# Optimization experiments

Measured on AMD Instinct MI355X. Metric: run time of the kernel, lower is better.

The kernel has to match this reference:

```python
import jax, jax.numpy as jnp
from jax import lax
import numpy as np

DIM = 512
NUM_HEADS = 8
SR = 2


def setup_inputs() -> dict:
    key = jax.random.key(0)
    ks = jax.random.split(key, 7)
    B, H, W = 4, 64, 64
    N = H * W
    C = DIM
    s = 0.02
    return {
        "x": jax.random.normal(ks[0], (B, N, C), dtype=jnp.float32),
        "q_w": jax.random.normal(ks[1], (C, C), dtype=jnp.float32) * s,
        "kv_w": jax.random.normal(ks[2], (2 * C, C), dtype=jnp.float32) * s,
        "sr_w": jax.random.normal(ks[3], (C, C, SR, SR), dtype=jnp.float32) * s,
        "sr_b": jax.random.normal(ks[4], (C,), dtype=jnp.float32) * s,
        "proj_w": jax.random.normal(ks[5], (C, C), dtype=jnp.float32) * s,
        "proj_b": jax.random.normal(ks[6], (C,), dtype=jnp.float32) * s,
        "H": H,
        "W": W,
    }


def reference(x, q_w, kv_w, sr_w, sr_b, proj_w, proj_b, H, W):
    B, N, C = x.shape
    nh = NUM_HEADS
    hd = C // nh
    scale = hd ** -0.5

    # q projection: [B, nh, N, hd]
    q = (x @ q_w.T).reshape(B, N, nh, hd).transpose(0, 2, 1, 3)

    # spatial reduction via strided conv (kernel=stride=SR)
    x_ = x.transpose(0, 2, 1).reshape(B, C, H, W)
    x_ = lax.conv_general_dilated(
        x_, sr_w, window_strides=(SR, SR), padding="VALID",
        dimension_numbers=("NCHW", "OIHW", "NCHW"),
    ) + sr_b[None, :, None, None]
    Nk = (H // SR) * (W // SR)
    x_ = x_.reshape(B, C, Nk).transpose(0, 2, 1)  # [B, Nk, C]

    # kv projection: [2, B, nh, Nk, hd]
    kv = (x_ @ kv_w.T).reshape(B, Nk, 2, nh, hd).transpose(2, 0, 3, 1, 4)
    k, v = kv[0], kv[1]

    attn = jax.nn.softmax(jnp.einsum("bhnd,bhmd->bhnm", q, k) * scale, axis=-1)
    out = jnp.einsum("bhnm,bhmd->bhnd", attn, v)  # [B, nh, N, hd]
    out = out.transpose(0, 2, 1, 3).reshape(B, N, C)
    return out @ proj_w.T + proj_b
```

## Files before the change

### kernel.cpp

```cpp
#include <hip/hip_runtime.h>


typedef __attribute__((ext_vector_type(8)))  short short8;
typedef __attribute__((ext_vector_type(8)))  unsigned short ushort8;
typedef __attribute__((ext_vector_type(4)))  float floatx4;
typedef __attribute__((ext_vector_type(16))) float floatx16;

__device__ inline unsigned short bf16r(float f) {
    union { float f; unsigned u; } v; v.f = f;
    unsigned r = v.u + 0x7fffu + ((v.u >> 16) & 1u);
    return (unsigned short)(r >> 16);
}

__device__ inline unsigned long long pack4ull(float4 v) {
    return (unsigned long long)bf16r(v.x)
         | ((unsigned long long)bf16r(v.y) << 16)
         | ((unsigned long long)bf16r(v.z) << 32)
         | ((unsigned long long)bf16r(v.w) << 48);
}

__device__ inline ushort8 pack8(float4 a, float4 b) {
    ushort8 o;
    o[0] = bf16r(a.x); o[1] = bf16r(a.y); o[2] = bf16r(a.z); o[3] = bf16r(a.w);
    o[4] = bf16r(b.x); o[5] = bf16r(b.y); o[6] = bf16r(b.z); o[7] = bf16r(b.w);
    return o;
}

__device__ inline void gl_lds16(const void* g, void* l) {
    __builtin_amdgcn_global_load_lds(
        (const __attribute__((address_space(1))) unsigned int*)g,
        (__attribute__((address_space(3))) unsigned int*)l, 16, 0, 0);
}

__global__ __launch_bounds__(256)
void prep(const float* __restrict__ x,  const float* __restrict__ qw,
          const float* __restrict__ kvw, const float* __restrict__ srw,
          const float* __restrict__ pw,
          unsigned short* __restrict__ xb,  unsigned short* __restrict__ qwb,
          unsigned short* __restrict__ kvwb, unsigned short* __restrict__ srwb,
          unsigned short* __restrict__ pwb, unsigned short* __restrict__ xrb) {
    const int bid = blockIdx.x;
    if (bid < 2048) {
        const int id = bid * 256 + threadIdx.x;
        const int cq = id & 127, m = id >> 7;
        const int c0 = cq * 4;
        const int b = m >> 10, rem = m & 1023;
        const int oi = rem >> 5, oj = rem & 31;
        const int n00 = oi * 128 + oj * 2;
        const float* bp = x + ((size_t)(b * 4096 + n00)) * 512 + c0;
        const float4 r00 = *(const float4*)bp;
        const float4 r01 = *(const float4*)(bp + 512);
        const float4 r10 = *(const float4*)(bp + 64 * 512);
        const float4 r11 = *(const float4*)(bp + 65 * 512);
        const unsigned long long w00 = pack4ull(r00), w01 = pack4ull(r01),
                                 w10 = pack4ull(r10), w11 = pack4ull(r11);
        unsigned short* xo = xb + ((size_t)(b * 4096 + n00)) * 512 + c0;
        *(unsigned long long*)(xo)            = w00;
        *(unsigned long long*)(xo + 512)      = w01;
        *(unsigned long long*)(xo + 64 * 512) = w10;
        *(unsigned long long*)(xo + 65 * 512) = w11;
        unsigned short* xd = xrb + (size_t)m * 2048 + c0 * 4;
        #pragma unroll
        for (int j = 0; j < 4; ++j) {
            const unsigned long long e =
                  ((w00 >> (16 * j)) & 0xffffull)
                | (((w01 >> (16 * j)) & 0xffffull) << 16)
                | (((w10 >> (16 * j)) & 0xffffull) << 32)
                | (((w11 >> (16 * j)) & 0xffffull) << 48);
            *(unsigned long long*)(xd + j * 4) = e;
        }
    } else {
        const int b2 = bid - 2048;
        const float* src; unsigned short* dst; int off; float sc = 1.f;
        if (b2 < 128)      { src = qw;  dst = qwb;  off = b2 * 256;
                             sc = 0.18033688011112042f;  }
        else if (b2 < 384) { src = kvw; dst = kvwb; off = (b2 - 128) * 256; }
        else if (b2 < 896) { src = srw; dst = srwb; off = (b2 - 384) * 256; }
        else               { src = pw;  dst = pwb;  off = (b2 - 896) * 256; }
        const int idx = off + threadIdx.x;
        float4 a = *(const float4*)(src + (size_t)idx * 8);
        float4 bq = *(const float4*)(src + (size_t)idx * 8 + 4);
        a.x *= sc; a.y *= sc; a.z *= sc; a.w *= sc;
        bq.x *= sc; bq.y *= sc; bq.z *= sc; bq.w *= sc;
        *(ushort8*)(dst + (size_t)idx * 8) = pack8(a, bq);
    }
}

__device__ __forceinline__ void g_stage64(
        const unsigned short* __restrict__ A, const unsigned short* __restrict__ B,
        int K, int bm, int bn, int k0, int t,
        unsigned short* AsB, unsigned short* BsB) {
    #pragma unroll
    for (int i = 0; i < 4; ++i) {
        const int c = i * 256 + t;
        const int r = c >> 3, ch = c & 7;
        gl_lds16(A + (size_t)(bm + r) * K + k0 + ((ch ^ (r & 7)) * 8), AsB + c * 8);
    }
    #pragma unroll
    for (int i = 0; i < 2; ++i) {
        const int c = i * 256 + t;
        const int r = c >> 3, ch = c & 7;
        gl_lds16(B + (size_t)(bn + r) * K + k0 + ((ch ^ (r & 7)) * 8), BsB + c * 8);
    }
}

__device__ __forceinline__ void g_comp64(
        const unsigned short* AsB, const unsigned short* BsB,
        int lq, int quad, int wrow, floatx4 (&acc)[2][4]) {
    short8 bf[2][4];
    #pragma unroll
    for (int kc = 0; kc < 2; ++kc)
        #pragma unroll
        for (int ni = 0; ni < 4; ++ni) {
            const int r = ni * 16 + lq;
            bf[kc][ni] = *(const short8*)&BsB[r * 64 + (((kc * 4 + quad) ^ (r & 7)) * 8)];
        }
    #pragma unroll
    for (int mi = 0; mi < 2; ++mi) {
        const int r = wrow + mi * 16 + lq;
        #pragma unroll
        for (int kc = 0; kc < 2; ++kc) {
            const short8 af = *(const short8*)&AsB[r * 64 + (((kc * 4 + quad) ^ (r & 7)) * 8)];
            #pragma unroll
            for (int ni = 0; ni < 4; ++ni)
                acc[mi][ni] = __builtin_amdgcn_mfma_f32_16x16x32_bf16(
                    af, bf[kc][ni], acc[mi][ni], 0, 0, 0);
        }
    }
}

__device__ __forceinline__ void g_run64(
        const unsigned short* __restrict__ A, const unsigned short* __restrict__ B,
        int K, int bm, int bn, int t, int lq, int quad, int wrow,
        unsigned short (&As)[2][128 * 64], unsigned short (&Bs)[2][64 * 64],
        floatx4 (&acc)[2][4]) {
    g_stage64(A, B, K, bm, bn, 0, t, As[0], Bs[0]);
    __syncthreads();
    const int nk = K >> 6;
    for (int ks = 0; ks < nk; ++ks) {
        const int cur = ks & 1;
        if (ks + 1 < nk)
            g_stage64(A, B, K, bm, bn, (ks + 1) * 64, t, As[cur ^ 1], Bs[cur ^ 1]);
        __builtin_amdgcn_s_setprio(1);
        g_comp64(As[cur], Bs[cur], lq, quad, wrow, acc);
        __builtin_amdgcn_s_setprio(0);
        if (ks + 1 < nk) __syncthreads();
    }
}

__global__ __launch_bounds__(256)
void gemm_qc(const unsigned short* __restrict__ xb, const unsigned short* __restrict__ qwb,
             const unsigned short* __restrict__ xrb, const unsigned short* __restrict__ srwb,
             const float* __restrict__ sr_b,
             unsigned short* __restrict__ qb, unsigned short* __restrict__ xsrb) {
    __shared__ unsigned short As[2][128 * 64];
    __shared__ unsigned short Bs[2][64 * 64];
    const int t = threadIdx.x;
    const int w = t >> 6, l = t & 63;
    const int lq = l & 15, quad = l >> 4;
    const int wrow = w * 32;
    const int bx = blockIdx.x;
    const unsigned short *A, *B; int K, bm; const float* bias; unsigned short* C;
    if (bx < 32) { A = xrb; B = srwb; K = 2048; bm = bx * 128;        bias = sr_b;    C = xsrb; }
    else         { A = xb;  B = qwb;  K = 512;  bm = (bx - 32) * 128; bias = nullptr; C = qb;   }
    const int bn = blockIdx.y * 64;

    floatx4 acc[2][4];
    #pragma unroll
    for (int mi = 0; mi < 2; ++mi)
        #pragma unroll
        for (int ni = 0; ni < 4; ++ni) acc[mi][ni] = (floatx4){0.f, 0.f, 0.f, 0.f};

    g_run64(A, B, K, bm, bn, t, lq, quad, wrow, As, Bs, acc);

    #pragma unroll
    for (int ni = 0; ni < 4; ++ni) {
        const int col = bn + ni * 16 + lq;
        const float bv = bias ? bias[col] : 0.f;
        #pragma unroll
        for (int mi = 0; mi < 2; ++mi) {
            const int row0 = bm + wrow + mi * 16 + quad * 4;
            unsigned own[4], mg[4];
            #pragma unroll
            for (int r = 0; r < 4; ++r) own[r] = bf16r(acc[mi][ni][r] + bv);
            #pragma unroll
            for (int r = 0; r < 4; ++r) {
                const unsigned pt = __shfl_xor(own[r], 1);
                mg[r] = (lq & 1) ? (pt | (own[r] << 16)) : (own[r] | (pt << 16));
            }
            const int colb = bn + ni * 16 + (lq & ~1);
            const int rb = (lq & 1) * 2;
            *(unsigned*)(C + (size_t)(row0 + rb)     * 512 + colb) = mg[rb];
            *(unsigned*)(C + (size_t)(row0 + rb + 1) * 512 + colb) = mg[rb + 1];
        }
    }
}

__global__ __launch_bounds__(256)
void gemm_kv(const unsigned short* __restrict__ kvwb, const unsigned short* __restrict__ xsrb,
             unsigned short* __restrict__ Kb, unsigned short* __restrict__ Vt) {
    __shared__ unsigned short As[2][128 * 64];
    __shared__ unsigned short Bs[2][64 * 64];
    const int t = threadIdx.x;
    const int w = t >> 6, l = t & 63;
    const int lq = l & 15, quad = l >> 4;
    const int wrow = w * 32;
    const int id = blockIdx.x;
    const bool isK = id < 256;
    const unsigned short* A = isK ? kvwb : xsrb;
    const unsigned short* B = isK ? xsrb : kvwb + (size_t)512 * 512;
    const int bm = isK ? (id & 3) * 128 : ((id - 256) >> 3) * 128;
    const int bn = isK ? (id >> 2) * 64 : ((id - 256) & 7) * 64;

    floatx4 acc[2][4];
    #pragma unroll
    for (int mi = 0; mi < 2; ++mi)
        #pragma unroll
        for (int ni = 0; ni < 4; ++ni) acc[mi][ni] = (floatx4){0.f, 0.f, 0.f, 0.f};

    g_run64(A, B, 512, bm, bn, t, lq, quad, wrow, As, Bs, acc);

    #pragma unroll
    for (int ni = 0; ni < 4; ++ni) {
        const int col = bn + ni * 16 + lq;
        #pragma unroll
        for (int mi = 0; mi < 2; ++mi) {
            const int row0 = bm + wrow + mi * 16 + quad * 4;
            unsigned long long wv = 0;
            #pragma unroll
            for (int r = 0; r < 4; ++r)
                wv |= (unsigned long long)bf16r(acc[mi][ni][r]) << (16 * r);
            if (isK) {
                const int kb = col >> 10, key = col & 1023;
                const int h = row0 >> 6, d0 = row0 & 63;
                *(unsigned long long*)(Kb +
                    (((size_t)(kb * 8 + h)) * 1024 + key) * 64 + d0) = wv;
            } else {
                const int kb = row0 >> 10, key0 = row0 & 1023;
                const int h = col >> 6, d = col & 63;
                *(unsigned long long*)(Vt +
                    (((size_t)(kb * 8 + h)) * 64 + d) * 1024 + key0) = wv;
            }
        }
    }
}

__global__ __launch_bounds__(256)
void gemm_proj(const unsigned short* __restrict__ attb, const unsigned short* __restrict__ pwb,
               const float* __restrict__ pb, float* __restrict__ out) {
    __shared__ unsigned short As[2][128 * 64];
    __shared__ unsigned short Bs[2][64 * 64];
    const int t = threadIdx.x;
    const int w = t >> 6, l = t & 63;
    const int lq = l & 15, quad = l >> 4;
    const int wrow = w * 32;
    const int bm = blockIdx.x * 128, bn = blockIdx.y * 64;

    floatx4 acc[2][4];
    #pragma unroll
    for (int mi = 0; mi < 2; ++mi)
        #pragma unroll
        for (int ni = 0; ni < 4; ++ni) acc[mi][ni] = (floatx4){0.f, 0.f, 0.f, 0.f};

    g_run64(attb, pwb, 512, bm, bn, t, lq, quad, wrow, As, Bs, acc);

    #pragma unroll
    for (int ni = 0; ni < 4; ++ni) {
        const int col = bn + ni * 16 + lq;
        const float bv = pb[col];
        #pragma unroll
        for (int mi = 0; mi < 2; ++mi) {
            const int row0 = bm + wrow + mi * 16 + quad * 4;
            #pragma unroll
            for (int r = 0; r < 4; ++r)
                out[(size_t)(row0 + r) * 512 + col] = acc[mi][ni][r] + bv;
        }
    }
}

#define KS2 72
#define VS2 136

__global__ __launch_bounds__(256)
void attn_mfma32(const unsigned short* __restrict__ qb,
                 const unsigned short* __restrict__ Kb,
                 const unsigned short* __restrict__ Vt,
                 unsigned short* __restrict__ out) {
    __shared__ unsigned short Ks[128 * KS2];
    __shared__ unsigned short Vs[64 * VS2];

    const int t = threadIdx.x;
    const int w = t >> 6;
    const int lane = t & 63;
    const int m32 = lane & 31;
    const int sig = lane >> 5;
    const int hw = blockIdx.x;
    const int lid = (hw & 7) * 128 + (hw >> 3);
    const int bh = lid >> 5;
    const int n0 = (lid & 31) * 128;
    const int b = bh >> 3, h = bh & 7;

    short8 qf[4];
    {
        const unsigned short* qrow =
            qb + ((size_t)(b * 4096 + n0 + w * 32 + m32)) * 512 + h * 64;
        #pragma unroll
        for (int kc = 0; kc < 4; ++kc)
            qf[kc] = *(const short8*)(qrow + kc * 16 + sig * 8);
    }

    float l_own = 0.f;
    floatx16 O0, O1;
    #pragma unroll
    for (int i = 0; i < 16; ++i) { O0[i] = 0.f; O1[i] = 0.f; }

    const unsigned short* Kg = Kb + (size_t)bh * 1024 * 64;
    const unsigned short* Vg = Vt + (size_t)bh * 64 * 1024;
    const int srow = t >> 2;
    const int sdb  = (t & 3) * 16;

    for (int kt2 = 0; kt2 < 8; ++kt2) {
        __syncthreads();
        {
            #pragma unroll
            for (int i = 0; i < 2; ++i) {
                const int row = i * 64 + srow;
                const unsigned short* src =
                    Kg + ((size_t)(kt2 * 128 + row)) * 64 + sdb;
                *(ushort8*)&Ks[row * KS2 + sdb]     = *(const ushort8*)src;
                *(ushort8*)&Ks[row * KS2 + sdb + 8] = *(const ushort8*)(src + 8);
            }
        }
        {
            #pragma unroll
            for (int i = 0; i < 2; ++i) {
                const int colb = i * 64 + sdb;
                const unsigned short* src =
                    Vg + (size_t)srow * 1024 + kt2 * 128 + colb;
                *(ushort8*)&Vs[srow * VS2 + colb]     = *(const ushort8*)src;
                *(ushort8*)&Vs[srow * VS2 + colb + 8] = *(const ushort8*)(src + 8);
            }
        }
        __syncthreads();

        #pragma unroll
        for (int half = 0; half < 2; ++half) {
            const int kof = half * 64;

            floatx16 st0, st1;
            #pragma unroll
            for (int i = 0; i < 16; ++i) { st0[i] = 0.f; st1[i] = 0.f; }
            __builtin_amdgcn_s_setprio(1);
            #pragma unroll
            for (int kc = 0; kc < 4; ++kc) {
                const short8 a0 = *(const short8*)
                    &Ks[(kof + m32) * KS2 + kc * 16 + sig * 8];
                st0 = __builtin_amdgcn_mfma_f32_32x32x16_bf16(a0, qf[kc], st0, 0, 0, 0);
                const short8 a1 = *(const short8*)
                    &Ks[(kof + 32 + m32) * KS2 + kc * 16 + sig * 8];
                st1 = __builtin_amdgcn_mfma_f32_32x32x16_bf16(a1, qf[kc], st1, 0, 0, 0);
            }
            __builtin_amdgcn_s_setprio(0);

            uint2 E[2][4];
            #pragma unroll
            for (int g = 0; g < 2; ++g) {
                #pragma unroll
                for (int qd = 0; qd < 4; ++qd) {
                    const float p0 = __builtin_amdgcn_exp2f(g ? st1[qd * 4 + 0] : st0[qd * 4 + 0]);
                    const float p1 = __builtin_amdgcn_exp2f(g ? st1[qd * 4 + 1] : st0[qd * 4 + 1]);
                    const float p2 = __builtin_amdgcn_exp2f(g ? st1[qd * 4 + 2] : st0[qd * 4 + 2]);
                    const float p3 = __builtin_amdgcn_exp2f(g ? st1[qd * 4 + 3] : st0[qd * 4 + 3]);
                    E[g][qd].x = __builtin_amdgcn_perm(
                        __float_as_uint(p1), __float_as_uint(p0), 0x07060302u);
                    E[g][qd].y = __builtin_amdgcn_perm(
                        __float_as_uint(p3), __float_as_uint(p2), 0x07060302u);
                    l_own += (p0 + p1) + (p2 + p3);
                }
            }

            __builtin_amdgcn_s_setprio(1);
            #pragma unroll
            for (int kc = 0; kc < 4; ++kc) {
                const int g = kc >> 1, qlo = (kc & 1) * 2;
                unsigned ax = E[g][qlo].x, bx_ = E[g][qlo + 1].x;
                unsigned ay = E[g][qlo].y, by_ = E[g][qlo + 1].y;
                asm("v_permlane32_swap_b32 %0, %1" : "+v"(ax), "+v"(bx_));
                asm("v_permlane32_swap_b32 %0, %1" : "+v"(ay), "+v"(by_));
                uint4 fr; fr.x = ax; fr.y = ay; fr.z = bx_; fr.w = by_;
                const short8 pa = *(const short8*)&fr;
                const short8 v0 = *(const short8*)
                    &Vs[m32 * VS2 + kof + kc * 16 + sig * 8];
                O0 = __builtin_amdgcn_mfma_f32_32x32x16_bf16(pa, v0, O0, 0, 0, 0);
                const short8 v1 = *(const short8*)
                    &Vs[(32 + m32) * VS2 + kof + kc * 16 + sig * 8];
                O1 = __builtin_amdgcn_mfma_f32_32x32x16_bf16(pa, v1, O1, 0, 0, 0);
            }
            __builtin_amdgcn_s_setprio(0);
        }
    }

    l_own += __shfl_xor(l_own, 32);
    const float inv = 1.0f / l_own;

    float fo0[16], fo1[16];
    #pragma unroll
    for (int r = 0; r < 16; ++r) {
        const float li = __shfl(inv, ((r & 3) + 8 * (r >> 2)) + 4 * sig);
        fo0[r] = O0[r] * li;
        fo1[r] = O1[r] * li;
    }

    #pragma unroll
    for (int gd = 0; gd < 2; ++gd) {
        unsigned mg[16];
        #pragma unroll
        for (int r = 0; r < 16; ++r) {
            const unsigned own = bf16r(gd ? fo1[r] : fo0[r]);
            const unsigned pt = __shfl_xor(own, 1);
            mg[r] = (m32 & 1) ? (pt | (own << 16)) : (own | (pt << 16));
        }
        if ((m32 & 1) == gd) {
            const int colb = h * 64 + gd * 32 + (m32 & ~1);
            #pragma unroll
            for (int r = 0; r < 16; ++r) {
                const int qrow = (r & 3) + 8 * (r >> 2) + 4 * sig;
                const size_t row = (size_t)(b * 4096 + n0 + w * 32 + qrow);
                *(unsigned*)(out + row * 512 + colb) = mg[r];
            }
        }
    }
}

extern "C" void kernel_launch(void* const* d_in, const int* in_sizes, int n_in,
                              void* d_out, int out_size, void* d_ws, size_t ws_size,
                              hipStream_t stream) {
    const float* x      = (const float*)d_in[0];
    const float* q_w    = (const float*)d_in[1];
    const float* kv_w   = (const float*)d_in[2];
    const float* sr_w   = (const float*)d_in[3];
    const float* sr_b   = (const float*)d_in[4];
    const float* proj_w = (const float*)d_in[5];
    const float* proj_b = (const float*)d_in[6];
    float* out = (float*)d_out;

    unsigned short* xb   = (unsigned short*)d_ws;
    unsigned short* attb = xb;
    unsigned short* qb   = xb   + (size_t)16384 * 512;
    unsigned short* xrb  = qb   + (size_t)16384 * 512;
    unsigned short* xsrb = xrb  + (size_t)4096 * 2048;
    unsigned short* qwb  = xsrb + (size_t)4096 * 512;
    unsigned short* kvwb = qwb  + (size_t)512 * 512;
    unsigned short* srwb = kvwb + (size_t)1024 * 512;
    unsigned short* pwb  = srwb + (size_t)512 * 2048;
    unsigned short* Kb   = pwb  + (size_t)512 * 512;
    unsigned short* Vt   = Kb   + (size_t)32 * 1024 * 64;

    const dim3 blk(256);

    prep<<<3072, blk, 0, stream>>>(x, q_w, kv_w, sr_w, proj_w,
                                   xb, qwb, kvwb, srwb, pwb, xrb);

    gemm_qc<<<dim3(160, 8), blk, 0, stream>>>(xb, qwb, xrb, srwb, sr_b, qb, xsrb);

    gemm_kv<<<512, blk, 0, stream>>>(kvwb, xsrb, Kb, Vt);

    attn_mfma32<<<1024, blk, 0, stream>>>(qb, Kb, Vt, attb);

    gemm_proj<<<dim3(128, 8), blk, 0, stream>>>(attb, pwb, proj_b, out);
}
```

Baseline: 216.9 us.

## Gather conv patches directly from bf16 x in GEMM loader instead of materializing xrb

Removes the separate im2col-style patch buffer (xrb) that prep wrote. The sr_w weights are instead reordered to a (kh,kw,c) K layout, and the conv GEMM's A-tile loader computes source rows in xb directly. This cuts a write and a re-read of 16 MB of bf16 patch data. In exchange, prep now does a simple flat conversion of x and a strided gather of sr_w, and the conv GEMM loads become less contiguous.

```diff
diff --git a/kernel.cpp b/kernel.cpp
--- a/kernel.cpp
+++ b/kernel.cpp
@@ -10,13 +10,6 @@
     union { float f; unsigned u; } v; v.f = f;
     unsigned r = v.u + 0x7fffu + ((v.u >> 16) & 1u);
     return (unsigned short)(r >> 16);
-}
-
-__device__ inline unsigned long long pack4ull(float4 v) {
-    return (unsigned long long)bf16r(v.x)
-         | ((unsigned long long)bf16r(v.y) << 16)
-         | ((unsigned long long)bf16r(v.z) << 32)
-         | ((unsigned long long)bf16r(v.w) << 48);
 }
 
 __device__ inline ushort8 pack8(float4 a, float4 b) {
@@ -38,45 +31,25 @@
           const float* __restrict__ pw,
           unsigned short* __restrict__ xb,  unsigned short* __restrict__ qwb,
           unsigned short* __restrict__ kvwb, unsigned short* __restrict__ srwb,
-          unsigned short* __restrict__ pwb, unsigned short* __restrict__ xrb) {
+          unsigned short* __restrict__ pwb) {
     const int bid = blockIdx.x;
-    if (bid < 2048) {
-        const int id = bid * 256 + threadIdx.x;
-        const int cq = id & 127, m = id >> 7;
-        const int c0 = cq * 4;
-        const int b = m >> 10, rem = m & 1023;
-        const int oi = rem >> 5, oj = rem & 31;
-        const int n00 = oi * 128 + oj * 2;
-        const float* bp = x + ((size_t)(b * 4096 + n00)) * 512 + c0;
-        const float4 r00 = *(const float4*)bp;
-        const float4 r01 = *(const float4*)(bp + 512);
-        const float4 r10 = *(const float4*)(bp + 64 * 512);
-        const float4 r11 = *(const float4*)(bp + 65 * 512);
-        const unsigned long long w00 = pack4ull(r00), w01 = pack4ull(r01),
-                                 w10 = pack4ull(r10), w11 = pack4ull(r11);
-        unsigned short* xo = xb + ((size_t)(b * 4096 + n00)) * 512 + c0;
-        *(unsigned long long*)(xo)            = w00;
-        *(unsigned long long*)(xo + 512)      = w01;
-        *(unsigned long long*)(xo + 64 * 512) = w10;
-        *(unsigned long long*)(xo + 65 * 512) = w11;
-        unsigned short* xd = xrb + (size_t)m * 2048 + c0 * 4;
-        #pragma unroll
-        for (int j = 0; j < 4; ++j) {
-            const unsigned long long e =
-                  ((w00 >> (16 * j)) & 0xffffull)
-                | (((w01 >> (16 * j)) & 0xffffull) << 16)
-                | (((w10 >> (16 * j)) & 0xffffull) << 32)
-                | (((w11 >> (16 * j)) & 0xffffull) << 48);
-            *(unsigned long long*)(xd + j * 4) = e;
-        }
+    if (bid >= 4480 && bid < 4992) {
+        const int idx = (bid - 4480) * 256 + threadIdx.x;
+        const int out8 = idx * 8;
+        const int o = out8 >> 11, rem = out8 & 2047;
+        const int j = rem >> 9, c0 = rem & 511;
+        const float* s = srw + (size_t)o * 2048 + c0 * 4 + j;
+        ushort8 v;
+        #pragma unroll
+        for (int k = 0; k < 8; ++k) v[k] = bf16r(s[k * 4]);
+        *(ushort8*)(srwb + (size_t)out8) = v;
     } else {
-        const int b2 = bid - 2048;
         const float* src; unsigned short* dst; int off; float sc = 1.f;
-        if (b2 < 128)      { src = qw;  dst = qwb;  off = b2 * 256;
-                             sc = 0.18033688011112042f;  }
-        else if (b2 < 384) { src = kvw; dst = kvwb; off = (b2 - 128) * 256; }
-        else if (b2 < 896) { src = srw; dst = srwb; off = (b2 - 384) * 256; }
-        else               { src = pw;  dst = pwb;  off = (b2 - 896) * 256; }
+        if (bid < 4096)      { src = x;   dst = xb;   off = bid * 256; }
+        else if (bid < 4224) { src = qw;  dst = qwb;  off = (bid - 4096) * 256;
+                               sc = 0.18033688011112042f;  }
+        else if (bid < 4480) { src = kvw; dst = kvwb; off = (bid - 4224) * 256; }
+        else                 { src = pw;  dst = pwb;  off = (bid - 4992) * 256; }
         const int idx = off + threadIdx.x;
         float4 a = *(const float4*)(src + (size_t)idx * 8);
         float4 bq = *(const float4*)(src + (size_t)idx * 8 + 4);
@@ -86,6 +59,7 @@
     }
 }
 
+template<bool CONV>
 __device__ __forceinline__ void g_stage64(
         const unsigned short* __restrict__ A, const unsigned short* __restrict__ B,
         int K, int bm, int bn, int k0, int t,
@@ -94,7 +68,17 @@
     for (int i = 0; i < 4; ++i) {
         const int c = i * 256 + t;
         const int r = c >> 3, ch = c & 7;
-        gl_lds16(A + (size_t)(bm + r) * K + k0 + ((ch ^ (r & 7)) * 8), AsB + c * 8);
+        const int kk = k0 + ((ch ^ (r & 7)) * 8);
+        if (CONV) {
+            const int m = bm + r;
+            const int bq = m >> 10, rem = m & 1023;
+            const int j = kk >> 9, cc = kk & 511;
+            const int row = bq * 4096 + (rem >> 5) * 128 + (rem & 31) * 2
+                            + (j >> 1) * 64 + (j & 1);
+            gl_lds16(A + (size_t)row * 512 + cc, AsB + c * 8);
+        } else {
+            gl_lds16(A + (size_t)(bm + r) * K + kk, AsB + c * 8);
+        }
     }
     #pragma unroll
     for (int i = 0; i < 2; ++i) {
@@ -129,18 +113,19 @@
     }
 }
 
+template<bool CONV>
 __device__ __forceinline__ void g_run64(
         const unsigned short* __restrict__ A, const unsigned short* __restrict__ B,
         int K, int bm, int bn, int t, int lq, int quad, int wrow,
         unsigned short (&As)[2][128 * 64], unsigned short (&Bs)[2][64 * 64],
         floatx4 (&acc)[2][4]) {
-    g_stage64(A, B, K, bm, bn, 0, t, As[0], Bs[0]);
+    g_stage64<CONV>(A, B, K, bm, bn, 0, t, As[0], Bs[0]);
     __syncthreads();
     const int nk = K >> 6;
     for (int ks = 0; ks < nk; ++ks) {
         const int cur = ks & 1;
         if (ks + 1 < nk)
-            g_stage64(A, B, K, bm, bn, (ks + 1) * 64, t, As[cur ^ 1], Bs[cur ^ 1]);
+            g_stage64<CONV>(A, B, K, bm, bn, (ks + 1) * 64, t, As[cur ^ 1], Bs[cur ^ 1]);
         __builtin_amdgcn_s_setprio(1);
         g_comp64(As[cur], Bs[cur], lq, quad, wrow, acc);
         __builtin_amdgcn_s_setprio(0);
@@ -150,7 +135,7 @@
 
 __global__ __launch_bounds__(256)
 void gemm_qc(const unsigned short* __restrict__ xb, const unsigned short* __restrict__ qwb,
-             const unsigned short* __restrict__ xrb, const unsigned short* __restrict__ srwb,
+             const unsigned short* __restrict__ srwb,
              const float* __restrict__ sr_b,
              unsigned short* __restrict__ qb, unsigned short* __restrict__ xsrb) {
     __shared__ unsigned short As[2][128 * 64];
@@ -160,9 +145,6 @@
     const int lq = l & 15, quad = l >> 4;
     const int wrow = w * 32;
     const int bx = blockIdx.x;
-    const unsigned short *A, *B; int K, bm; const float* bias; unsigned short* C;
-    if (bx < 32) { A = xrb; B = srwb; K = 2048; bm = bx * 128;        bias = sr_b;    C = xsrb; }
-    else         { A = xb;  B = qwb;  K = 512;  bm = (bx - 32) * 128; bias = nullptr; C = qb;   }
     const int bn = blockIdx.y * 64;
 
     floatx4 acc[2][4];
@@ -171,7 +153,16 @@
         #pragma unroll
         for (int ni = 0; ni < 4; ++ni) acc[mi][ni] = (floatx4){0.f, 0.f, 0.f, 0.f};
 
-    g_run64(A, B, K, bm, bn, t, lq, quad, wrow, As, Bs, acc);
+    const float* bias; unsigned short* C; int bm;
+    if (bx < 32) {
+        bm = bx * 128;
+        g_run64<true>(xb, srwb, 2048, bm, bn, t, lq, quad, wrow, As, Bs, acc);
+        bias = sr_b; C = xsrb;
+    } else {
+        bm = (bx - 32) * 128;
+        g_run64<false>(xb, qwb, 512, bm, bn, t, lq, quad, wrow, As, Bs, acc);
+        bias = nullptr; C = qb;
+    }
 
     #pragma unroll
     for (int ni = 0; ni < 4; ++ni) {
@@ -218,7 +209,7 @@
         #pragma unroll
         for (int ni = 0; ni < 4; ++ni) acc[mi][ni] = (floatx4){0.f, 0.f, 0.f, 0.f};
 
-    g_run64(A, B, 512, bm, bn, t, lq, quad, wrow, As, Bs, acc);
+    g_run64<false>(A, B, 512, bm, bn, t, lq, quad, wrow, As, Bs, acc);
 
     #pragma unroll
     for (int ni = 0; ni < 4; ++ni) {
@@ -262,7 +253,7 @@
         #pragma unroll
         for (int ni = 0; ni < 4; ++ni) acc[mi][ni] = (floatx4){0.f, 0.f, 0.f, 0.f};
 
-    g_run64(attb, pwb, 512, bm, bn, t, lq, quad, wrow, As, Bs, acc);
+    g_run64<false>(attb, pwb, 512, bm, bn, t, lq, quad, wrow, As, Bs, acc);
 
     #pragma unroll
     for (int ni = 0; ni < 4; ++ni) {
@@ -447,8 +438,7 @@
     unsigned short* xb   = (unsigned short*)d_ws;
     unsigned short* attb = xb;
     unsigned short* qb   = xb   + (size_t)16384 * 512;
-    unsigned short* xrb  = qb   + (size_t)16384 * 512;
-    unsigned short* xsrb = xrb  + (size_t)4096 * 2048;
+    unsigned short* xsrb = qb   + (size_t)16384 * 512;
     unsigned short* qwb  = xsrb + (size_t)4096 * 512;
     unsigned short* kvwb = qwb  + (size_t)512 * 512;
     unsigned short* srwb = kvwb + (size_t)1024 * 512;
@@ -458,10 +448,10 @@
 
     const dim3 blk(256);
 
-    prep<<<3072, blk, 0, stream>>>(x, q_w, kv_w, sr_w, proj_w,
-                                   xb, qwb, kvwb, srwb, pwb, xrb);
-
-    gemm_qc<<<dim3(160, 8), blk, 0, stream>>>(xb, qwb, xrb, srwb, sr_b, qb, xsrb);
+    prep<<<5120, blk, 0, stream>>>(x, q_w, kv_w, sr_w, proj_w,
+                                   xb, qwb, kvwb, srwb, pwb);
+
+    gemm_qc<<<dim3(160, 8), blk, 0, stream>>>(xb, qwb, srwb, sr_b, qb, xsrb);
 
     gemm_kv<<<512, blk, 0, stream>>>(kvwb, xsrb, Kb, Vt);
 
```

Measured after the change: 219.4 us. No clear change (+1.1%).
